# Kernel optimization log

Hardware: AMD Instinct MI355X
Metric: run time of the kernel (lower is better)

Reference implementation:

```python
import jax, jax.numpy as jnp
import numpy as np

B = 1048576

def _mlp3(x, W1, b1, W2, b2, W3, b3):
    # x: [..., d] -> [..., 1]; Linear(d,d)+ReLU, Linear(d,d)+ReLU, Linear(d,1)
    h = jax.nn.relu(jnp.einsum('...d,od->...o', x, W1) + b1)
    h = jax.nn.relu(jnp.einsum('...d,od->...o', h, W2) + b2)
    return jnp.einsum('...d,od->...o', h, W3) + b3

def setup_inputs() -> dict:
    key = jax.random.key(0)
    ks = jax.random.split(key, 20)
    def lin(k, out_d, in_d):
        bound = 1.0 / np.sqrt(in_d)
        k1, k2 = jax.random.split(k)
        W = jax.random.uniform(k1, (out_d, in_d), jnp.float32, -bound, bound)
        b = jax.random.uniform(k2, (out_d,), jnp.float32, -bound, bound)
        return W, b
    inp = {
        'edge': jax.random.normal(ks[0], (B, 4, 10), jnp.float32),
        'cross': jax.random.normal(ks[1], (B, 4, 8), jnp.float32),
        'corner': jax.random.normal(ks[2], (B, 4, 10), jnp.float32),
        'cn': jax.random.normal(ks[3], (B, 1), jnp.float32),
    }
    eW1, eb1 = lin(ks[4], 10, 10); eW2, eb2 = lin(ks[5], 10, 10); eW3, eb3 = lin(ks[6], 1, 10)
    xW1, xb1 = lin(ks[7], 8, 8);  xW2, xb2 = lin(ks[8], 8, 8);  xW3, xb3 = lin(ks[9], 1, 8)
    cW1, cb1 = lin(ks[10], 10, 10); cW2, cb2 = lin(ks[11], 10, 10); cW3, cb3 = lin(ks[12], 1, 10)
    nW, nb = lin(ks[13], 1, 1)
    inp.update(dict(eW1=eW1, eb1=eb1, eW2=eW2, eb2=eb2, eW3=eW3, eb3=eb3,
                    xW1=xW1, xb1=xb1, xW2=xW2, xb2=xb2, xW3=xW3, xb3=xb3,
                    cW1=cW1, cb1=cb1, cW2=cW2, cb2=cb2, cW3=cW3, cb3=cb3,
                    nW=nW, nb=nb))
    return inp

def reference(edge, cross, corner, cn,
              eW1, eb1, eW2, eb2, eW3, eb3,
              xW1, xb1, xW2, xb2, xW3, xb3,
              cW1, cb1, cW2, cb2, cW3, cb3,
              nW, nb) -> jnp.ndarray:
    # Shared-weight MLP over each of the 4 slices, summed over the slice dim.
    e = _mlp3(edge, eW1, eb1, eW2, eb2, eW3, eb3).sum(axis=1)    # [B,1]
    x = _mlp3(cross, xW1, xb1, xW2, xb2, xW3, xb3).sum(axis=1)   # [B,1]
    c = _mlp3(corner, cW1, cb1, cW2, cb2, cW3, cb3).sum(axis=1)  # [B,1]
    n = jnp.einsum('bd,od->bo', cn, nW) + nb                     # [B,1]
    return e + x + c + n
```

## Files before the change

kernel.cpp:

```cpp
#include <hip/hip_runtime.h>


typedef float f2 __attribute__((ext_vector_type(2)));

template<int D>
__device__ __forceinline__ float mlp_slice(const f2* xs,
                                           const float* __restrict__ W1,
                                           const float* __restrict__ b1,
                                           const float* __restrict__ W2,
                                           const float* __restrict__ b2,
                                           const float* __restrict__ W3,
                                           const float* __restrict__ b3)
{
    constexpr int H = D / 2;

    f2 h1[H];
    #pragma unroll
    for (int op = 0; op < H; ++op) {
        f2 a = {b1[2 * op], b1[2 * op + 1]};
        #pragma unroll
        for (int i = 0; i < D; ++i) {
            const float xv = (i & 1) ? xs[i >> 1].y : xs[i >> 1].x;
            const f2 w = {W1[(2 * op) * D + i], W1[(2 * op + 1) * D + i]};
            a = __builtin_elementwise_fma(w, (f2){xv, xv}, a);
        }
        h1[op] = __builtin_elementwise_max(a, (f2){0.0f, 0.0f});
    }

    f2 h2[H];
    #pragma unroll
    for (int op = 0; op < H; ++op) {
        f2 a = {b2[2 * op], b2[2 * op + 1]};
        #pragma unroll
        for (int i = 0; i < D; ++i) {
            const float hv = (i & 1) ? h1[i >> 1].y : h1[i >> 1].x;
            const f2 w = {W2[(2 * op) * D + i], W2[(2 * op + 1) * D + i]};
            a = __builtin_elementwise_fma(w, (f2){hv, hv}, a);
        }
        h2[op] = __builtin_elementwise_max(a, (f2){0.0f, 0.0f});
    }

    f2 o = {0.0f, 0.0f};
    #pragma unroll
    for (int k = 0; k < H; ++k) {
        const f2 w3 = {W3[2 * k], W3[2 * k + 1]};
        o = __builtin_elementwise_fma(w3, h2[k], o);
    }
    return o.x + o.y + b3[0];
}

__global__ __launch_bounds__(256)
void osero_kernel(const float* __restrict__ edge,
                  const float* __restrict__ cross_,
                  const float* __restrict__ corner,
                  const float* __restrict__ cn,
                  const float* __restrict__ eW1, const float* __restrict__ eb1,
                  const float* __restrict__ eW2, const float* __restrict__ eb2,
                  const float* __restrict__ eW3, const float* __restrict__ eb3,
                  const float* __restrict__ xW1, const float* __restrict__ xb1,
                  const float* __restrict__ xW2, const float* __restrict__ xb2,
                  const float* __restrict__ xW3, const float* __restrict__ xb3,
                  const float* __restrict__ cW1, const float* __restrict__ cb1,
                  const float* __restrict__ cW2, const float* __restrict__ cb2,
                  const float* __restrict__ cW3, const float* __restrict__ cb3,
                  const float* __restrict__ nW,  const float* __restrict__ nb,
                  float* __restrict__ out, int nelem)
{
    const int g = blockIdx.x * 256 + threadIdx.x;
    const int e = g >> 2;
    const int s = g & 3;
    if (e >= nelem) return;

    f2 xe[5];
    {
        const f2* p = reinterpret_cast<const f2*>(edge) + (size_t)g * 5;
        #pragma unroll
        for (int k = 0; k < 5; ++k) xe[k] = p[k];
    }
    f2 xq[5];
    {
        const f2* p = reinterpret_cast<const f2*>(corner) + (size_t)g * 5;
        #pragma unroll
        for (int k = 0; k < 5; ++k) xq[k] = p[k];
    }
    f2 xc[4];
    {
        const float4* p = reinterpret_cast<const float4*>(cross_) + (size_t)g * 2;
        const float4 v0 = p[0];
        const float4 v1 = p[1];
        xc[0] = (f2){v0.x, v0.y}; xc[1] = (f2){v0.z, v0.w};
        xc[2] = (f2){v1.x, v1.y}; xc[3] = (f2){v1.z, v1.w};
    }
    const float cnv = (s == 0) ? cn[e] : 0.0f;

    float val = mlp_slice<10>(xe, eW1, eb1, eW2, eb2, eW3, eb3);
    val      += mlp_slice<10>(xq, cW1, cb1, cW2, cb2, cW3, cb3);
    val      += mlp_slice<8> (xc, xW1, xb1, xW2, xb2, xW3, xb3);

    val += __shfl_xor(val, 1, 4);
    val += __shfl_xor(val, 2, 4);

    if (s == 0)
        out[e] = val + fmaf(cnv, nW[0], nb[0]);
}

extern "C" void kernel_launch(void* const* d_in, const int* in_sizes, int n_in,
                              void* d_out, int out_size, void* d_ws, size_t ws_size,
                              hipStream_t stream) {
    const float* edge   = (const float*)d_in[0];
    const float* cross_ = (const float*)d_in[1];
    const float* corner = (const float*)d_in[2];
    const float* cn     = (const float*)d_in[3];
    const float* eW1 = (const float*)d_in[4];
    const float* eb1 = (const float*)d_in[5];
    const float* eW2 = (const float*)d_in[6];
    const float* eb2 = (const float*)d_in[7];
    const float* eW3 = (const float*)d_in[8];
    const float* eb3 = (const float*)d_in[9];
    const float* xW1 = (const float*)d_in[10];
    const float* xb1 = (const float*)d_in[11];
    const float* xW2 = (const float*)d_in[12];
    const float* xb2 = (const float*)d_in[13];
    const float* xW3 = (const float*)d_in[14];
    const float* xb3 = (const float*)d_in[15];
    const float* cW1 = (const float*)d_in[16];
    const float* cb1 = (const float*)d_in[17];
    const float* cW2 = (const float*)d_in[18];
    const float* cb2 = (const float*)d_in[19];
    const float* cW3 = (const float*)d_in[20];
    const float* cb3 = (const float*)d_in[21];
    const float* nW  = (const float*)d_in[22];
    const float* nb  = (const float*)d_in[23];

    const int nelem = in_sizes[3];
    const int nthr  = nelem * 4;
    const int nblk  = (nthr + 255) / 256;

    osero_kernel<<<dim3(nblk), 256, 0, stream>>>(edge, cross_, corner, cn,
                                                 eW1, eb1, eW2, eb2, eW3, eb3,
                                                 xW1, xb1, xW2, xb2, xW3, xb3,
                                                 cW1, cb1, cW2, cb2, cW3, cb3,
                                                 nW, nb, (float*)d_out, nelem);
}
```

Before: 460.1 us.

## Process four elements per thread with weights staged in shared memory

Each thread now computes four strided batch elements, reusing each packed weight pair across all four instead of reloading it per element. Weights and biases are preloaded once per block into shared memory as pre-paired f2 values. This targets per-element weight-load overhead at the cost of higher register pressure and a launch that assumes the batch is a multiple of 1024 with no bounds check.

```diff
diff --git a/kernel.cpp b/kernel.cpp
--- a/kernel.cpp
+++ b/kernel.cpp
@@ -3,50 +3,88 @@
 
 typedef float f2 __attribute__((ext_vector_type(2)));
 
+__device__ __forceinline__ f2 pk_fma(f2 a, f2 b, f2 c) {
+    return __builtin_elementwise_fma(a, b, c);
+}
+
+__device__ __forceinline__ f2 pr10(const float* __restrict__ W, int j) {
+    const int op = j / 10, i = j - op * 10;
+    return (f2){W[op * 20 + i], W[op * 20 + 10 + i]};
+}
+__device__ __forceinline__ f2 pr8(const float* __restrict__ W, int j) {
+    const int op = j >> 3, i = j & 7;
+    return (f2){W[op * 16 + i], W[op * 16 + 8 + i]};
+}
+__device__ __forceinline__ f2 prc(const float* __restrict__ p, int k) {
+    return (f2){p[2 * k], p[2 * k + 1]};
+}
+
+struct SW {
+    f2 eW1[50], eW2[50], cW1[50], cW2[50];
+    f2 xW1[32], xW2[32];
+    f2 eW3[5], cW3[5], xW3[4];
+    f2 eb1[5], eb2[5], cb1[5], cb2[5];
+    f2 xb1[4], xb2[4];
+};
+
 template<int D>
-__device__ __forceinline__ float mlp_slice(const f2* xs,
-                                           const float* __restrict__ W1,
-                                           const float* __restrict__ b1,
-                                           const float* __restrict__ W2,
-                                           const float* __restrict__ b2,
-                                           const float* __restrict__ W3,
-                                           const float* __restrict__ b3)
+__device__ __forceinline__ void mlp_quad(const f2 (&xs)[4][D / 2],
+                                         const f2* __restrict__ w1p, const f2* __restrict__ b1p,
+                                         const f2* __restrict__ w2p, const f2* __restrict__ b2p,
+                                         const f2* __restrict__ w3p, const float b3v,
+                                         float (&val)[4])
 {
     constexpr int H = D / 2;
 
-    f2 h1[H];
+    f2 h1[4][H];
     #pragma unroll
     for (int op = 0; op < H; ++op) {
-        f2 a = {b1[2 * op], b1[2 * op + 1]};
+        const f2 b = b1p[op];
+        f2 a[4] = {b, b, b, b};
         #pragma unroll
         for (int i = 0; i < D; ++i) {
-            const float xv = (i & 1) ? xs[i >> 1].y : xs[i >> 1].x;
-            const f2 w = {W1[(2 * op) * D + i], W1[(2 * op + 1) * D + i]};
-            a = __builtin_elementwise_fma(w, (f2){xv, xv}, a);
-        }
-        h1[op] = __builtin_elementwise_max(a, (f2){0.0f, 0.0f});
-    }
-
-    f2 h2[H];
+            const f2 w = w1p[op * D + i];
+            #pragma unroll
+            for (int e = 0; e < 4; ++e) {
+                const float xv = (i & 1) ? xs[e][i >> 1].y : xs[e][i >> 1].x;
+                a[e] = pk_fma(w, (f2){xv, xv}, a[e]);
+            }
+        }
+        #pragma unroll
+        for (int e = 0; e < 4; ++e)
+            h1[e][op] = __builtin_elementwise_max(a[e], (f2){0.0f, 0.0f});
+    }
+
+    f2 h2[4][H];
     #pragma unroll
     for (int op = 0; op < H; ++op) {
-        f2 a = {b2[2 * op], b2[2 * op + 1]};
+        const f2 b = b2p[op];
+        f2 a[4] = {b, b, b, b};
         #pragma unroll
         for (int i = 0; i < D; ++i) {
-            const float hv = (i & 1) ? h1[i >> 1].y : h1[i >> 1].x;
-            const f2 w = {W2[(2 * op) * D + i], W2[(2 * op + 1) * D + i]};
-            a = __builtin_elementwise_fma(w, (f2){hv, hv}, a);
-        }
-        h2[op] = __builtin_elementwise_max(a, (f2){0.0f, 0.0f});
-    }
-
-    f2 o = {0.0f, 0.0f};
+            const f2 w = w2p[op * D + i];
+            #pragma unroll
+            for (int e = 0; e < 4; ++e) {
+                const float hv = (i & 1) ? h1[e][i >> 1].y : h1[e][i >> 1].x;
+                a[e] = pk_fma(w, (f2){hv, hv}, a[e]);
+            }
+        }
+        #pragma unroll
+        for (int e = 0; e < 4; ++e)
+            h2[e][op] = __builtin_elementwise_max(a[e], (f2){0.0f, 0.0f});
+    }
+
+    f2 o[4] = {{0.f, 0.f}, {0.f, 0.f}, {0.f, 0.f}, {0.f, 0.f}};
     #pragma unroll
     for (int k = 0; k < H; ++k) {
-        const f2 w3 = {W3[2 * k], W3[2 * k + 1]};
-        o = __builtin_elementwise_fma(w3, h2[k], o);
-    }
-    return o.x + o.y + b3[0];
+        const f2 w3 = w3p[k];
+        #pragma unroll
+        for (int e = 0; e < 4; ++e)
+            o[e] = pk_fma(w3, h2[e][k], o[e]);
+    }
+    #pragma unroll
+    for (int e = 0; e < 4; ++e)
+        val[e] += o[e].x + o[e].y + b3v;
 }
 
 __global__ __launch_bounds__(256)
@@ -64,44 +102,83 @@
                   const float* __restrict__ cW2, const float* __restrict__ cb2,
                   const float* __restrict__ cW3, const float* __restrict__ cb3,
                   const float* __restrict__ nW,  const float* __restrict__ nb,
-                  float* __restrict__ out, int nelem)
+                  float* __restrict__ out, int q )
 {
-    const int g = blockIdx.x * 256 + threadIdx.x;
-    const int e = g >> 2;
-    const int s = g & 3;
-    if (e >= nelem) return;
-
-    f2 xe[5];
+    __shared__ SW sw;
+    const int t = threadIdx.x;
+
+    if (t < 50) {
+        sw.eW1[t] = pr10(eW1, t); sw.eW2[t] = pr10(eW2, t);
+        sw.cW1[t] = pr10(cW1, t); sw.cW2[t] = pr10(cW2, t);
+    } else if (t >= 64 && t < 96) {
+        const int j = t - 64;
+        sw.xW1[j] = pr8(xW1, j); sw.xW2[j] = pr8(xW2, j);
+    } else if (t >= 128 && t < 133) {
+        const int k = t - 128;
+        sw.eW3[k] = prc(eW3, k); sw.cW3[k] = prc(cW3, k);
+        sw.eb1[k] = prc(eb1, k); sw.eb2[k] = prc(eb2, k);
+        sw.cb1[k] = prc(cb1, k); sw.cb2[k] = prc(cb2, k);
+    } else if (t >= 192 && t < 196) {
+        const int k = t - 192;
+        sw.xW3[k] = prc(xW3, k);
+        sw.xb1[k] = prc(xb1, k); sw.xb2[k] = prc(xb2, k);
+    }
+    __syncthreads();
+
+    const int g = blockIdx.x * 256 + t;
+    const int s = t & 3;
+    float val[4] = {0.f, 0.f, 0.f, 0.f};
+
     {
-        const f2* p = reinterpret_cast<const f2*>(edge) + (size_t)g * 5;
-        #pragma unroll
-        for (int k = 0; k < 5; ++k) xe[k] = p[k];
-    }
-    f2 xq[5];
+        f2 xs[4][5];
+        #pragma unroll
+        for (int k = 0; k < 4; ++k) {
+            const f2* p = reinterpret_cast<const f2*>(edge)
+                        + (size_t)g * 5 + (size_t)k * q * 20;
+            #pragma unroll
+            for (int j = 0; j < 5; ++j) xs[k][j] = p[j];
+        }
+        mlp_quad<10>(xs, sw.eW1, sw.eb1, sw.eW2, sw.eb2, sw.eW3, eb3[0], val);
+    }
     {
-        const f2* p = reinterpret_cast<const f2*>(corner) + (size_t)g * 5;
-        #pragma unroll
-        for (int k = 0; k < 5; ++k) xq[k] = p[k];
-    }
-    f2 xc[4];
+        f2 xs[4][5];
+        #pragma unroll
+        for (int k = 0; k < 4; ++k) {
+            const f2* p = reinterpret_cast<const f2*>(corner)
+                        + (size_t)g * 5 + (size_t)k * q * 20;
+            #pragma unroll
+            for (int j = 0; j < 5; ++j) xs[k][j] = p[j];
+        }
+        mlp_quad<10>(xs, sw.cW1, sw.cb1, sw.cW2, sw.cb2, sw.cW3, cb3[0], val);
+    }
     {
-        const float4* p = reinterpret_cast<const float4*>(cross_) + (size_t)g * 2;
-        const float4 v0 = p[0];
-        const float4 v1 = p[1];
-        xc[0] = (f2){v0.x, v0.y}; xc[1] = (f2){v0.z, v0.w};
-        xc[2] = (f2){v1.x, v1.y}; xc[3] = (f2){v1.z, v1.w};
-    }
-    const float cnv = (s == 0) ? cn[e] : 0.0f;
-
-    float val = mlp_slice<10>(xe, eW1, eb1, eW2, eb2, eW3, eb3);
-    val      += mlp_slice<10>(xq, cW1, cb1, cW2, cb2, cW3, cb3);
-    val      += mlp_slice<8> (xc, xW1, xb1, xW2, xb2, xW3, xb3);
-
-    val += __shfl_xor(val, 1, 4);
-    val += __shfl_xor(val, 2, 4);
-
-    if (s == 0)
-        out[e] = val + fmaf(cnv, nW[0], nb[0]);
+        f2 xs[4][4];
+        #pragma unroll
+        for (int k = 0; k < 4; ++k) {
+            const float4* p = reinterpret_cast<const float4*>(cross_)
+                            + (size_t)g * 2 + (size_t)k * q * 8;
+            const float4 v0 = p[0];
+            const float4 v1 = p[1];
+            xs[k][0] = (f2){v0.x, v0.y}; xs[k][1] = (f2){v0.z, v0.w};
+            xs[k][2] = (f2){v1.x, v1.y}; xs[k][3] = (f2){v1.z, v1.w};
+        }
+        mlp_quad<8>(xs, sw.xW1, sw.xb1, sw.xW2, sw.xb2, sw.xW3, xb3[0], val);
+    }
+
+    #pragma unroll
+    for (int k = 0; k < 4; ++k) {
+        val[k] += __shfl_xor(val[k], 1, 4);
+        val[k] += __shfl_xor(val[k], 2, 4);
+    }
+    if (s == 0) {
+        const float w0 = nW[0], b0 = nb[0];
+        const int e0 = g >> 2;
+        #pragma unroll
+        for (int k = 0; k < 4; ++k) {
+            const int e = e0 + k * q;
+            out[e] = val[k] + fmaf(cn[e], w0, b0);
+        }
+    }
 }
 
 extern "C" void kernel_launch(void* const* d_in, const int* in_sizes, int n_in,
@@ -133,12 +210,12 @@
     const float* nb  = (const float*)d_in[23];
 
     const int nelem = in_sizes[3];
-    const int nthr  = nelem * 4;
-    const int nblk  = (nthr + 255) / 256;
+    const int q     = nelem / 4;
+    const int nblk  = nelem / 256;
 
     osero_kernel<<<dim3(nblk), 256, 0, stream>>>(edge, cross_, corner, cn,
                                                  eW1, eb1, eW2, eb2, eW3, eb3,
                                                  xW1, xb1, xW2, xb2, xW3, xb3,
                                                  cW1, cb1, cW2, cb2, cW3, cb3,
-                                                 nW, nb, (float*)d_out, nelem);
-}
+                                                 nW, nb, (float*)d_out, q);
+}
```

After: 456.3 us. About the same (-0.8%).

## Stage interleaved MLP weights in shared memory and issue input loads first

Applied to the files above, without the earlier changes.

Each block now copies all three MLPs' weights and biases into LDS, pre-paired as float2 row pairs, so the packed FMAs read one aligned pair per step. The input loads are issued before the weight staging, with a scheduling barrier to keep that order, so their latency overlaps the copy. The last-layer bias is folded into a single tail term, and launch bounds now request 6 blocks per SM. The cost is a block-wide barrier and extra LDS traffic in place of scalar or broadcast global loads of uniform weights, which may already have been cheap.

```diff
diff --git a/kernel.cpp b/kernel.cpp
--- a/kernel.cpp
+++ b/kernel.cpp
@@ -3,26 +3,46 @@
 
 typedef float f2 __attribute__((ext_vector_type(2)));
 
+__device__ __forceinline__ f2 pk_fma(f2 a, f2 b, f2 c) {
+    return __builtin_elementwise_fma(a, b, c);
+}
+
+__device__ __forceinline__ f2 pr10(const float* __restrict__ W, int j) {
+    const int op = j / 10, i = j - op * 10;
+    return (f2){W[op * 20 + i], W[op * 20 + 10 + i]};
+}
+__device__ __forceinline__ f2 pr8(const float* __restrict__ W, int j) {
+    const int op = j >> 3, i = j & 7;
+    return (f2){W[op * 16 + i], W[op * 16 + 8 + i]};
+}
+__device__ __forceinline__ f2 prc(const float* __restrict__ p, int k) {
+    return (f2){p[2 * k], p[2 * k + 1]};
+}
+
+struct SW {
+    f2 eW1[50], eW2[50], cW1[50], cW2[50];
+    f2 xW1[32], xW2[32];
+    f2 eW3[5], cW3[5], xW3[4];
+    f2 eb1[5], eb2[5], cb1[5], cb2[5];
+    f2 xb1[4], xb2[4];
+};
+
 template<int D>
 __device__ __forceinline__ float mlp_slice(const f2* xs,
-                                           const float* __restrict__ W1,
-                                           const float* __restrict__ b1,
-                                           const float* __restrict__ W2,
-                                           const float* __restrict__ b2,
-                                           const float* __restrict__ W3,
-                                           const float* __restrict__ b3)
+                                           const f2* w1p, const f2* b1p,
+                                           const f2* w2p, const f2* b2p,
+                                           const f2* w3p)
 {
     constexpr int H = D / 2;
 
     f2 h1[H];
     #pragma unroll
     for (int op = 0; op < H; ++op) {
-        f2 a = {b1[2 * op], b1[2 * op + 1]};
+        f2 a = b1p[op];
         #pragma unroll
         for (int i = 0; i < D; ++i) {
             const float xv = (i & 1) ? xs[i >> 1].y : xs[i >> 1].x;
-            const f2 w = {W1[(2 * op) * D + i], W1[(2 * op + 1) * D + i]};
-            a = __builtin_elementwise_fma(w, (f2){xv, xv}, a);
+            a = pk_fma(w1p[op * D + i], (f2){xv, xv}, a);
         }
         h1[op] = __builtin_elementwise_max(a, (f2){0.0f, 0.0f});
     }
@@ -30,26 +50,23 @@
     f2 h2[H];
     #pragma unroll
     for (int op = 0; op < H; ++op) {
-        f2 a = {b2[2 * op], b2[2 * op + 1]};
+        f2 a = b2p[op];
         #pragma unroll
         for (int i = 0; i < D; ++i) {
             const float hv = (i & 1) ? h1[i >> 1].y : h1[i >> 1].x;
-            const f2 w = {W2[(2 * op) * D + i], W2[(2 * op + 1) * D + i]};
-            a = __builtin_elementwise_fma(w, (f2){hv, hv}, a);
+            a = pk_fma(w2p[op * D + i], (f2){hv, hv}, a);
         }
         h2[op] = __builtin_elementwise_max(a, (f2){0.0f, 0.0f});
     }
 
     f2 o = {0.0f, 0.0f};
     #pragma unroll
-    for (int k = 0; k < H; ++k) {
-        const f2 w3 = {W3[2 * k], W3[2 * k + 1]};
-        o = __builtin_elementwise_fma(w3, h2[k], o);
-    }
-    return o.x + o.y + b3[0];
+    for (int k = 0; k < H; ++k)
+        o = pk_fma(w3p[k], h2[k], o);
+    return o.x + o.y;
 }
 
-__global__ __launch_bounds__(256)
+__global__ __launch_bounds__(256, 6)
 void osero_kernel(const float* __restrict__ edge,
                   const float* __restrict__ cross_,
                   const float* __restrict__ corner,
@@ -64,44 +81,62 @@
                   const float* __restrict__ cW2, const float* __restrict__ cb2,
                   const float* __restrict__ cW3, const float* __restrict__ cb3,
                   const float* __restrict__ nW,  const float* __restrict__ nb,
-                  float* __restrict__ out, int nelem)
+                  float* __restrict__ out, int nthr)
 {
-    const int g = blockIdx.x * 256 + threadIdx.x;
-    const int e = g >> 2;
-    const int s = g & 3;
-    if (e >= nelem) return;
+    __shared__ SW sw;
+    const int t = threadIdx.x;
+    const int g0 = blockIdx.x * 256 + t;
+    const int g  = (g0 < nthr) ? g0 : 0;
+    const int e  = g >> 2;
+    const int s  = g & 3;
 
-    f2 xe[5];
+    f2 xe[5], xq[5], xc[4];
     {
-        const f2* p = reinterpret_cast<const f2*>(edge) + (size_t)g * 5;
+        const f2* pe = reinterpret_cast<const f2*>(edge)   + (size_t)g * 5;
+        const f2* pq = reinterpret_cast<const f2*>(corner) + (size_t)g * 5;
         #pragma unroll
-        for (int k = 0; k < 5; ++k) xe[k] = p[k];
-    }
-    f2 xq[5];
-    {
-        const f2* p = reinterpret_cast<const f2*>(corner) + (size_t)g * 5;
+        for (int k = 0; k < 5; ++k) xe[k] = pe[k];
         #pragma unroll
-        for (int k = 0; k < 5; ++k) xq[k] = p[k];
-    }
-    f2 xc[4];
-    {
-        const float4* p = reinterpret_cast<const float4*>(cross_) + (size_t)g * 2;
-        const float4 v0 = p[0];
-        const float4 v1 = p[1];
+        for (int k = 0; k < 5; ++k) xq[k] = pq[k];
+        const float4* pc = reinterpret_cast<const float4*>(cross_) + (size_t)g * 2;
+        const float4 v0 = pc[0];
+        const float4 v1 = pc[1];
         xc[0] = (f2){v0.x, v0.y}; xc[1] = (f2){v0.z, v0.w};
         xc[2] = (f2){v1.x, v1.y}; xc[3] = (f2){v1.z, v1.w};
     }
     const float cnv = (s == 0) ? cn[e] : 0.0f;
+    __builtin_amdgcn_sched_barrier(0);
 
-    float val = mlp_slice<10>(xe, eW1, eb1, eW2, eb2, eW3, eb3);
-    val      += mlp_slice<10>(xq, cW1, cb1, cW2, cb2, cW3, cb3);
-    val      += mlp_slice<8> (xc, xW1, xb1, xW2, xb2, xW3, xb3);
+    if (t < 50) {
+        sw.eW1[t] = pr10(eW1, t); sw.eW2[t] = pr10(eW2, t);
+        sw.cW1[t] = pr10(cW1, t); sw.cW2[t] = pr10(cW2, t);
+    } else if (t >= 64 && t < 96) {
+        const int j = t - 64;
+        sw.xW1[j] = pr8(xW1, j); sw.xW2[j] = pr8(xW2, j);
+    } else if (t >= 128 && t < 133) {
+        const int k = t - 128;
+        sw.eW3[k] = prc(eW3, k); sw.cW3[k] = prc(cW3, k);
+        sw.eb1[k] = prc(eb1, k); sw.eb2[k] = prc(eb2, k);
+        sw.cb1[k] = prc(cb1, k); sw.cb2[k] = prc(cb2, k);
+    } else if (t >= 192 && t < 196) {
+        const int k = t - 192;
+        sw.xW3[k] = prc(xW3, k);
+        sw.xb1[k] = prc(xb1, k); sw.xb2[k] = prc(xb2, k);
+    }
+    __syncthreads();
+
+    float val = mlp_slice<10>(xe, sw.eW1, sw.eb1, sw.eW2, sw.eb2, sw.eW3);
+    val      += mlp_slice<10>(xq, sw.cW1, sw.cb1, sw.cW2, sw.cb2, sw.cW3);
+    val      += mlp_slice<8> (xc, sw.xW1, sw.xb1, sw.xW2, sw.xb2, sw.xW3);
 
     val += __shfl_xor(val, 1, 4);
     val += __shfl_xor(val, 2, 4);
 
-    if (s == 0)
-        out[e] = val + fmaf(cnv, nW[0], nb[0]);
+    if (s == 0 && g0 < nthr) {
+        const float tail = 4.0f * (eb3[0] + cb3[0] + xb3[0])
+                         + fmaf(cnv, nW[0], nb[0]);
+        out[e] = val + tail;
+    }
 }
 
 extern "C" void kernel_launch(void* const* d_in, const int* in_sizes, int n_in,
@@ -140,5 +175,5 @@
                                                  eW1, eb1, eW2, eb2, eW3, eb3,
                                                  xW1, xb1, xW2, xb2, xW3, xb3,
                                                  cW1, cb1, cW2, cb2, cW3, cb3,
-                                                 nW, nb, (float*)d_out, nelem);
+                                                 nW, nb, (float*)d_out, nthr);
 }
```

Result: no change. 460.7 us (+0.1%).
